# Performance work log

Hardware: AMD Instinct MI355X
Metric: run time of the kernel (lower is better)

The kernel has to match this reference:

```python
import jax, jax.numpy as jnp
import numpy as np

N_LAYERS = 3


def setup_inputs() -> dict:
    key = jax.random.key(0)
    k1, k2, k3, k4 = jax.random.split(key, 4)
    user_emb = jax.random.normal(k1, (29858, 64), dtype=jnp.float32)
    item_emb = jax.random.normal(k2, (40981, 64), dtype=jnp.float32)
    v = jax.random.normal(k3, (70839, 512), dtype=jnp.float32)
    filters = jax.random.normal(k4, (N_LAYERS, 512), dtype=jnp.float32)
    return {"user_emb": user_emb, "item_emb": item_emb, "v": v, "filters": filters}


def reference(user_emb, item_emb, v, filters):
    # ego: [N, D], v: [N, F], filters: [L, F]
    n_users = user_emb.shape[0]
    ego = jnp.concatenate([user_emb, item_emb], axis=0)
    acc = ego  # running sum for the mean over (layers + 1) embeddings
    for k in range(filters.shape[0]):
        # V @ diag(f) @ V^T @ ego  ==  V @ (f[:, None] * (V^T @ ego))
        proj = v.T @ ego                      # [F, D]
        ego = v @ (filters[k][:, None] * proj)  # [N, D]
        acc = acc + ego
    all_emb = acc / (filters.shape[0] + 1)
    return all_emb[:n_users], all_emb[n_users:]
```

## Files before the change

kernel.cpp:

```cpp
#include <hip/hip_runtime.h>
#include <hip/hip_bf16.h>


#define N_USERS 29858
#define N_TOTAL 70839
#define DQ 64
#define FD 512
#define NPAD 71168

typedef __attribute__((ext_vector_type(8))) short short8;
typedef __attribute__((ext_vector_type(4))) short short4v;
typedef __attribute__((ext_vector_type(4))) float f32x4;
typedef unsigned int u32;
typedef unsigned short u16;

static __device__ __forceinline__ u32 f32u(float x){union{float f;u32 u;}a;a.f=x;return a.u;}
static __device__ __forceinline__ float uf32(u32 u){union{u32 u;float f;}a;a.u=u;return a.f;}
static __device__ __forceinline__ u32 pack_h(u32 x0, u32 x1){
  return __builtin_amdgcn_perm(x1, x0, 0x07060302u);
}
static __device__ __forceinline__ void split_pair(u32 x0, u32 x1, u32& hp, u32& lp) {
  hp = pack_h(x0, x1);
  u32 l0 = f32u(uf32(x0) - uf32(x0 & 0xFFFF0000u));
  u32 l1 = f32u(uf32(x1) - uf32(x1 & 0xFFFF0000u));
  lp = pack_h(l0, l1);
}
union U8x { u32 u[4]; short8 s; };

static __device__ __forceinline__ u16 bf16_rne(float x) {
  u32 u = f32u(x);
  return (u16)((u + 0x7FFFu + ((u >> 16) & 1u)) >> 16);
}
static __device__ __forceinline__ void split2(float x, u16& h, u16& l) {
  h = bf16_rne(x);
  l = bf16_rne(x - uf32(((u32)h) << 16));
}

static __device__ __forceinline__ void load_lds16(const float* g, float* l) {
  __builtin_amdgcn_global_load_lds(
      (const __attribute__((address_space(1))) u32*)(g),
      (__attribute__((address_space(3))) u32*)(l), 16, 0, 0);
}


__global__ __launch_bounds__(256) void init_kernel(
    const float* __restrict__ u, const float* __restrict__ it,
    float* __restrict__ out, u16* __restrict__ egoTb) {
  __shared__ float tile[64][65];
  const int n0 = blockIdx.x * 64;
  const int t = threadIdx.x;
  const int r = t >> 2, cbase = (t & 3) * 16;
  {
    int n = n0 + r;
    if (n < N_TOTAL) {
      const float* src = (n < N_USERS) ? (u + (size_t)n * DQ)
                                       : (it + (size_t)(n - N_USERS) * DQ);
#pragma unroll
      for (int q = 0; q < 4; ++q) {
        f32x4 val = *(const f32x4*)(src + cbase + q * 4);
        *(f32x4*)(out + (size_t)n * DQ + cbase + q * 4) = val;
        tile[r][cbase + q * 4 + 0] = val[0];
        tile[r][cbase + q * 4 + 1] = val[1];
        tile[r][cbase + q * 4 + 2] = val[2];
        tile[r][cbase + q * 4 + 3] = val[3];
      }
    } else {
#pragma unroll
      for (int q = 0; q < 4; ++q)
#pragma unroll
        for (int e = 0; e < 4; ++e) tile[r][cbase + q * 4 + e] = 0.f;
    }
  }
  __syncthreads();
  const int s = t;
  const int d = (s & 15) | ((s >> 6) << 4);
  const int nb = (s >> 4) & 3;
#pragma unroll
  for (int sl = 0; sl < 2; ++sl) {
    U8x H, L;
#pragma unroll
    for (int j = 0; j < 4; ++j) {
      u16 h0, l0, h1, l1;
      split2(tile[sl * 32 + nb * 8 + 2 * j][d], h0, l0);
      split2(tile[sl * 32 + nb * 8 + 2 * j + 1][d], h1, l1);
      H.u[j] = (u32)h0 | ((u32)h1 << 16);
      L.u[j] = (u32)l0 | ((u32)l1 << 16);
    }
    size_t base = (size_t)(blockIdx.x * 2 + sl) * 4096;
    *(short8*)(egoTb + base + (size_t)s * 8) = H.s;
    *(short8*)(egoTb + base + 2048 + (size_t)s * 8) = L.s;
  }
}

__global__ __launch_bounds__(256, 3) void gram_kernel(
    const float* __restrict__ v, const u16* __restrict__ egoTb,
    float* __restrict__ parts, int chunk) {
  __shared__ short8 HAh[1024];
  __shared__ short8 HAl[1024];
  __shared__ short8 HBh[256];
  __shared__ short8 HBl[256];

  const int lid = blockIdx.x;
  const int cidx = (lid & 7) + 8 * ((lid >> 3) / 14);
  const int job = (lid >> 3) % 14;
  const int n0c = cidx * chunk;
  if (n0c >= NPAD) return;
  const int nend = min(n0c + chunk, NPAD);
  const bool isC0 = (job >= 12);
  const int itile = isC0 ? (job - 12) : (job < 8 ? 0 : 1);
  const int fA = itile * 256;
  const int jcol = isC0 ? 0 : (job < 8 ? job : job - 4);
  const int colbase = jcol * 64;
  const bool reuseB = !isC0 && (colbase >= fA) && (colbase + 64 <= fA + 256);
  const bool stageB = !isC0 && !reuseB;
  const int cb0q = reuseB ? ((colbase - fA) >> 6) : 0;

  const int t = threadIdx.x;
  const int lane = t & 63, wv = t >> 6;
  const int m16 = lane & 15, quad = lane >> 4;
  const int fl = lane, nq = wv;

  f32x4 acc[4][4];
#pragma unroll
  for (int a = 0; a < 4; ++a)
#pragma unroll
    for (int b = 0; b < 4; ++b) acc[a][b] = (f32x4){0.f, 0.f, 0.f, 0.f};

  u32 xA[4][8];
  u32 xB[8];
  short8 xBh, xBl;

  auto issue = [&](int n0) {
    if (isC0) {
      xBh = *(const short8*)(egoTb + (size_t)(n0 >> 5) * 4096 + (size_t)t * 8);
      xBl = *(const short8*)(egoTb + (size_t)(n0 >> 5) * 4096 + 2048 + (size_t)t * 8);
    }
#pragma unroll
    for (int seg = 0; seg < 4; ++seg)
#pragma unroll
      for (int r = 0; r < 8; ++r) {
        int n = n0 + nq * 8 + r;
        xA[seg][r] = (n < N_TOTAL) ? f32u(v[(size_t)n * FD + fA + seg * 64 + fl]) : 0u;
      }
    if (stageB) {
#pragma unroll
      for (int r = 0; r < 8; ++r) {
        int n = n0 + nq * 8 + r;
        xB[r] = (n < N_TOTAL) ? f32u(v[(size_t)n * FD + colbase + fl]) : 0u;
      }
    }
  };

  issue(n0c);

  for (int n0 = n0c; n0 < nend; n0 += 32) {
    asm volatile("s_barrier" ::: "memory");

    const int uw = (fl & 15) + ((fl >> 4) & 3) * 64 + nq * 16;
#pragma unroll
    for (int seg = 0; seg < 4; ++seg) {
      U8x H, L;
#pragma unroll
      for (int p = 0; p < 4; ++p)
        split_pair(xA[seg][2 * p], xA[seg][2 * p + 1], H.u[p], L.u[p]);
      HAh[uw + seg * 256] = H.s;
      HAl[uw + seg * 256] = L.s;
    }
    if (stageB) {
      U8x H, L;
#pragma unroll
      for (int p = 0; p < 4; ++p)
        split_pair(xB[2 * p], xB[2 * p + 1], H.u[p], L.u[p]);
      HBh[uw] = H.s;
      HBl[uw] = L.s;
    } else if (isC0) {
      HBh[t] = xBh;
      HBl[t] = xBl;
    }

    if (n0 + 32 < nend) issue(n0 + 32);

    asm volatile("s_waitcnt lgkmcnt(0)" ::: "memory");
    asm volatile("s_barrier" ::: "memory");

    short8 ah[4], al[4];
#pragma unroll
    for (int mt = 0; mt < 4; ++mt) {
      int u = m16 + mt * 64 + wv * 256 + quad * 16;
      ah[mt] = HAh[u];
      al[mt] = HAl[u];
    }
#pragma unroll
    for (int ct = 0; ct < 4; ++ct) {
      short8 bh, bl;
      if (reuseB) {
        int u = m16 + ct * 64 + cb0q * 256 + quad * 16;
        bh = HAh[u]; bl = HAl[u];
      } else {
        int u = m16 + ct * 64 + quad * 16;
        bh = HBh[u]; bl = HBl[u];
      }
#pragma unroll
      for (int mt = 0; mt < 4; ++mt) {
        acc[mt][ct] = __builtin_amdgcn_mfma_f32_16x16x32_bf16(ah[mt], bh, acc[mt][ct], 0, 0, 0);
        acc[mt][ct] = __builtin_amdgcn_mfma_f32_16x16x32_bf16(ah[mt], bl, acc[mt][ct], 0, 0, 0);
        acc[mt][ct] = __builtin_amdgcn_mfma_f32_16x16x32_bf16(al[mt], bh, acc[mt][ct], 0, 0, 0);
      }
    }
  }

  float* pb = parts + (size_t)cidx * (512 * 576);
  const int cb = isC0 ? 512 : colbase;
#pragma unroll
  for (int mt = 0; mt < 4; ++mt) {
    int row = fA + wv * 64 + mt * 16 + quad * 4;
#pragma unroll
    for (int ct = 0; ct < 4; ++ct) {
      int col = cb + ct * 16 + m16;
#pragma unroll
      for (int reg = 0; reg < 4; ++reg)
        pb[(size_t)(row + reg) * 576 + col] = acc[mt][ct][reg];
    }
  }
}

__global__ __launch_bounds__(256) void finalize_kernel(
    const float* __restrict__ parts, int nc,
    float* __restrict__ G, float* __restrict__ c0) {
  int idx = blockIdx.x * 256 + threadIdx.x;
  int r = idx / 576, c = idx % 576;
  float s = 0.f;
  if (c >= 512) {
    for (int p = 0; p < nc; ++p) s += parts[(size_t)p * (512 * 576) + r * 576 + c];
    c0[r * 64 + (c - 512)] = s;
  } else {
    bool direct = (c >> 6) >= 4 * (r >> 8);
    int rr = direct ? r : c, cc = direct ? c : r;
    for (int p = 0; p < nc; ++p) s += parts[(size_t)p * (512 * 576) + rr * 576 + cc];
    G[r * 512 + c] = s;
  }
}

__global__ __launch_bounds__(256) void apply_g_kernel(
    const float* __restrict__ G, const float* __restrict__ filt,
    const float* __restrict__ cin, float* __restrict__ cout) {
  __shared__ float red[4][64];
  const int t = threadIdx.x;
  const int i = blockIdx.x;
  const int sub = t >> 6, d = t & 63;
  float s = 0.f;
#pragma unroll 8
  for (int j = sub * 128; j < (sub + 1) * 128; ++j)
    s += G[i * 512 + j] * (filt[j] * cin[j * 64 + d]);
  red[sub][d] = s;
  __syncthreads();
  if (sub == 0)
    cout[i * 64 + d] = red[0][d] + red[1][d] + red[2][d] + red[3][d];
}

__global__ __launch_bounds__(256) void prep_wt_kernel(
    const float* __restrict__ filters, const float* __restrict__ c0,
    const float* __restrict__ c1, const float* __restrict__ c2,
    u16* __restrict__ wt_h) {
  int idx = blockIdx.x * 256 + threadIdx.x;
  int d = idx >> 9, f = idx & 511;
  float w = filters[f] * c0[f * 64 + d] + filters[512 + f] * c1[f * 64 + d] +
            filters[1024 + f] * c2[f * 64 + d];
  wt_h[d * FD + f] = bf16_rne(w);
}

__global__ __launch_bounds__(256) void expand_kernel(
    const float* __restrict__ v, const u16* __restrict__ wt_h,
    float* __restrict__ out) {
  __shared__ float raw[2][128 * 64];
  const int t = threadIdx.x;
  const int lane = t & 63, wv = t >> 6;
  const int m16 = lane & 15, quad = lane >> 4;
  const int nb = blockIdx.x * 128;

  f32x4 acc[2][4];
#pragma unroll
  for (int a = 0; a < 2; ++a)
#pragma unroll
    for (int b = 0; b < 4; ++b) acc[a][b] = (f32x4){0.f, 0.f, 0.f, 0.f};

  auto stage = [&](int buf, int fs) {
#pragma unroll
    for (int g = 0; g < 8; ++g) {
      int rl = g * 4 + (lane >> 4);
      int sw = rl & 7;
      int grow = min(nb + wv * 32 + rl, N_TOTAL - 1);
      const float* gp = v + (size_t)grow * FD + fs + (((lane & 15) ^ sw) << 2);
      load_lds16(gp, &raw[buf][(wv * 32 + g * 4) * 64]);
    }
  };

  stage(0, 0);
  for (int it8 = 0; it8 < 8; ++it8) {
    const int buf = it8 & 1, fs = it8 * 64;
    short8 pbh[2][4];
#pragma unroll
    for (int k = 0; k < 2; ++k)
#pragma unroll
      for (int ct = 0; ct < 4; ++ct) {
        const size_t off = (size_t)(ct * 16 + m16) * FD + fs + k * 32 + quad * 8;
        pbh[k][ct] = *(const short8*)(wt_h + off);
      }
    asm volatile("" ::: "memory");
    if (it8 + 1 < 8) {
      stage(buf ^ 1, fs + 64);
      asm volatile("s_waitcnt vmcnt(16)" ::: "memory");
    } else {
      asm volatile("s_waitcnt vmcnt(8)" ::: "memory");
    }
#pragma unroll
    for (int k0i = 0; k0i < 2; ++k0i) {
      short8 ah[2];
#pragma unroll
      for (int mt = 0; mt < 2; ++mt) {
        const float* rb = &raw[buf][(wv * 32 + mt * 16 + m16) * 64];
        const int sw = m16 & 7;
        const int j0 = k0i * 8 + quad * 2;
        f32x4 xa = *(const f32x4*)(rb + ((j0 ^ sw) << 2));
        f32x4 xb = *(const f32x4*)(rb + (((j0 + 1) ^ sw) << 2));
        U8x H;
        H.u[0] = pack_h(f32u(xa[0]), f32u(xa[1]));
        H.u[1] = pack_h(f32u(xa[2]), f32u(xa[3]));
        H.u[2] = pack_h(f32u(xb[0]), f32u(xb[1]));
        H.u[3] = pack_h(f32u(xb[2]), f32u(xb[3]));
        ah[mt] = H.s;
      }
#pragma unroll
      for (int ct = 0; ct < 4; ++ct) {
#pragma unroll
        for (int mt = 0; mt < 2; ++mt) {
          acc[mt][ct] = __builtin_amdgcn_mfma_f32_16x16x32_bf16(ah[mt], pbh[k0i][ct], acc[mt][ct], 0, 0, 0);
        }
      }
    }
  }

#pragma unroll
  for (int mt = 0; mt < 2; ++mt) {
    int nrow = nb + wv * 32 + mt * 16 + quad * 4;
#pragma unroll
    for (int ct = 0; ct < 4; ++ct) {
      int d = ct * 16 + m16;
#pragma unroll
      for (int reg = 0; reg < 4; ++reg) {
        int n = nrow + reg;
        if (n < N_TOTAL) {
          float* op = out + (size_t)n * DQ + d;
          *op = (*op + acc[mt][ct][reg]) * 0.25f;
        }
      }
    }
  }
}

extern "C" void kernel_launch(void* const* d_in, const int* in_sizes, int n_in,
                              void* d_out, int out_size, void* d_ws, size_t ws_size,
                              hipStream_t stream) {
  const float* user_emb = (const float*)d_in[0];
  const float* item_emb = (const float*)d_in[1];
  const float* v        = (const float*)d_in[2];
  const float* filters  = (const float*)d_in[3];
  float* out = (float*)d_out;

  const size_t EGOTB_BYTES = (size_t)(NPAD / 32) * 8192;
  const size_t SMALL_BYTES = (512 * 512 + 3 * 512 * 64) * 4 + DQ * FD * 2;
  size_t avail = ws_size > EGOTB_BYTES + SMALL_BYTES
                     ? ws_size - EGOTB_BYTES - SMALL_BYTES : 0;
  int nc = (int)(avail / ((size_t)512 * 576 * 4));
  if (nc > 35) nc = 35;
  if (nc < 1) nc = 1;
  int chunk = ((NPAD + nc - 1) / nc + 31) & ~31;
  int ncA = (NPAD + chunk - 1) / chunk;

  u16* egoTb  = (u16*)d_ws;
  float* parts = (float*)((char*)d_ws + EGOTB_BYTES);
  float* G     = parts + (size_t)ncA * 512 * 576;
  float* c0    = G + 512 * 512;
  float* c1    = c0 + 512 * 64;
  float* c2    = c1 + 512 * 64;
  u16* wt_h    = (u16*)(c2 + 512 * 64);

  int gblocks = 8 * 14 * ((ncA + 7) / 8);

  init_kernel<<<NPAD / 64, 256, 0, stream>>>(user_emb, item_emb, out, egoTb);
  gram_kernel<<<gblocks, 256, 0, stream>>>(v, egoTb, parts, chunk);
  finalize_kernel<<<(512 * 576) / 256, 256, 0, stream>>>(parts, ncA, G, c0);
  apply_g_kernel<<<512, 256, 0, stream>>>(G, filters, c0, c1);
  apply_g_kernel<<<512, 256, 0, stream>>>(G, filters + 512, c1, c2);
  prep_wt_kernel<<<128, 256, 0, stream>>>(filters, c0, c1, c2, wt_h);
  expand_kernel<<<NPAD / 128, 256, 0, stream>>>(v, wt_h, out);
}
```

Before: 486.8 us.

## Presplit V into bf16 hi/lo tiles once before the Gram kernel

Adds a presplit kernel that converts V once into bf16 high and low halves, stored in the MFMA-ready tiled layout. The Gram kernel then loads those tiles with vector loads instead of redoing scalar fp32 loads and splits for every job. This removes redundant split ALU work and the strided scalar loads, since each V segment was read by several jobs. In exchange it writes and reads an extra pass over a 2-byte-per-element copy of V (about 146MB total), needs a large workspace (falling back to the old path otherwise), and changes the grid mapping and occupancy hint.

```diff
diff --git a/kernel.cpp b/kernel.cpp
--- a/kernel.cpp
+++ b/kernel.cpp
@@ -9,7 +9,6 @@
 #define NPAD 71168
 
 typedef __attribute__((ext_vector_type(8))) short short8;
-typedef __attribute__((ext_vector_type(4))) short short4v;
 typedef __attribute__((ext_vector_type(4))) float f32x4;
 typedef unsigned int u32;
 typedef unsigned short u16;
@@ -72,9 +71,8 @@
     }
   }
   __syncthreads();
-  const int s = t;
-  const int d = (s & 15) | ((s >> 6) << 4);
-  const int nb = (s >> 4) & 3;
+  const int d = (t & 15) | ((t >> 6) << 4);
+  const int nb = (t >> 4) & 3;
 #pragma unroll
   for (int sl = 0; sl < 2; ++sl) {
     U8x H, L;
@@ -87,24 +85,67 @@
       L.u[j] = (u32)l0 | ((u32)l1 << 16);
     }
     size_t base = (size_t)(blockIdx.x * 2 + sl) * 4096;
-    *(short8*)(egoTb + base + (size_t)s * 8) = H.s;
-    *(short8*)(egoTb + base + 2048 + (size_t)s * 8) = L.s;
-  }
-}
-
-__global__ __launch_bounds__(256, 3) void gram_kernel(
-    const float* __restrict__ v, const u16* __restrict__ egoTb,
-    float* __restrict__ parts, int chunk) {
+    *(short8*)(egoTb + base + (size_t)t * 8) = H.s;
+    *(short8*)(egoTb + base + 2048 + (size_t)t * 8) = L.s;
+  }
+}
+
+__global__ __launch_bounds__(256) void presplit_kernel(
+    const float* __restrict__ v, u16* __restrict__ vbh, u16* __restrict__ vbl) {
+  __shared__ float tile[64][65];
+  const int n0 = blockIdx.x * 64;
+  const int t = threadIdx.x;
+  const int r = t >> 2, cbase = (t & 3) * 16;
+  const int d = (t & 15) | ((t >> 6) << 4);
+  const int nb = (t >> 4) & 3;
+  for (int fo = 0; fo < FD; fo += 64) {
+    __syncthreads();
+    {
+      int n = n0 + r;
+      if (n < N_TOTAL) {
+        const float* src = v + (size_t)n * FD + fo;
+#pragma unroll
+        for (int q = 0; q < 4; ++q) {
+          f32x4 val = *(const f32x4*)(src + cbase + q * 4);
+          tile[r][cbase + q * 4 + 0] = val[0];
+          tile[r][cbase + q * 4 + 1] = val[1];
+          tile[r][cbase + q * 4 + 2] = val[2];
+          tile[r][cbase + q * 4 + 3] = val[3];
+        }
+      } else {
+#pragma unroll
+        for (int q = 0; q < 4; ++q)
+#pragma unroll
+          for (int e = 0; e < 4; ++e) tile[r][cbase + q * 4 + e] = 0.f;
+      }
+    }
+    __syncthreads();
+#pragma unroll
+    for (int sl = 0; sl < 2; ++sl) {
+      U8x H, L;
+#pragma unroll
+      for (int j = 0; j < 4; ++j) {
+        u32 x0 = f32u(tile[sl * 32 + nb * 8 + 2 * j][d]);
+        u32 x1 = f32u(tile[sl * 32 + nb * 8 + 2 * j + 1][d]);
+        split_pair(x0, x1, H.u[j], L.u[j]);
+      }
+      size_t T = (size_t)((n0 >> 5) + sl) * 8 + (fo >> 6);
+      *(short8*)(vbh + T * 2048 + (size_t)t * 8) = H.s;
+      *(short8*)(vbl + T * 2048 + (size_t)t * 8) = L.s;
+    }
+  }
+}
+
+__global__ __launch_bounds__(256, 2) void gram_fast_kernel(
+    const u16* __restrict__ vbh, const u16* __restrict__ vbl,
+    const u16* __restrict__ egoTb, float* __restrict__ parts, int chunk) {
   __shared__ short8 HAh[1024];
   __shared__ short8 HAl[1024];
   __shared__ short8 HBh[256];
   __shared__ short8 HBl[256];
 
-  const int lid = blockIdx.x;
-  const int cidx = (lid & 7) + 8 * ((lid >> 3) / 14);
-  const int job = (lid >> 3) % 14;
-  const int n0c = cidx * chunk;
-  if (n0c >= NPAD) return;
+  const int job = blockIdx.x;
+  const int n0c = blockIdx.y * chunk;
   const int nend = min(n0c + chunk, NPAD);
   const bool isC0 = (job >= 12);
   const int itile = isC0 ? (job - 12) : (job < 8 ? 0 : 1);
@@ -118,7 +159,7 @@
   const int t = threadIdx.x;
   const int lane = t & 63, wv = t >> 6;
   const int m16 = lane & 15, quad = lane >> 4;
-  const int fl = lane, nq = wv;
+  const int ftA = fA >> 6;
 
   f32x4 acc[4][4];
 #pragma unroll
@@ -126,28 +167,23 @@
 #pragma unroll
     for (int b = 0; b < 4; ++b) acc[a][b] = (f32x4){0.f, 0.f, 0.f, 0.f};
 
-  u32 xA[4][8];
-  u32 xB[8];
-  short8 xBh, xBl;
+  short8 xAh[4], xAl[4], xBh, xBl;
 
   auto issue = [&](int n0) {
+    size_t Tb = (size_t)(n0 >> 5) * 8;
     if (isC0) {
       xBh = *(const short8*)(egoTb + (size_t)(n0 >> 5) * 4096 + (size_t)t * 8);
       xBl = *(const short8*)(egoTb + (size_t)(n0 >> 5) * 4096 + 2048 + (size_t)t * 8);
-    }
-#pragma unroll
-    for (int seg = 0; seg < 4; ++seg)
-#pragma unroll
-      for (int r = 0; r < 8; ++r) {
-        int n = n0 + nq * 8 + r;
-        xA[seg][r] = (n < N_TOTAL) ? f32u(v[(size_t)n * FD + fA + seg * 64 + fl]) : 0u;
-      }
-    if (stageB) {
-#pragma unroll
-      for (int r = 0; r < 8; ++r) {
-        int n = n0 + nq * 8 + r;
-        xB[r] = (n < N_TOTAL) ? f32u(v[(size_t)n * FD + colbase + fl]) : 0u;
-      }
+    } else if (stageB) {
+      size_t base = (Tb + (colbase >> 6)) * 2048 + (size_t)t * 8;
+      xBh = *(const short8*)(vbh + base);
+      xBl = *(const short8*)(vbl + base);
+    }
+#pragma unroll
+    for (int seg = 0; seg < 4; ++seg) {
+      size_t base = (Tb + ftA + seg) * 2048 + (size_t)t * 8;
+      xAh[seg] = *(const short8*)(vbh + base);
+      xAl[seg] = *(const short8*)(vbl + base);
     }
   };
 
@@ -156,24 +192,12 @@
   for (int n0 = n0c; n0 < nend; n0 += 32) {
     asm volatile("s_barrier" ::: "memory");
 
-    const int uw = (fl & 15) + ((fl >> 4) & 3) * 64 + nq * 16;
 #pragma unroll
     for (int seg = 0; seg < 4; ++seg) {
-      U8x H, L;
-#pragma unroll
-      for (int p = 0; p < 4; ++p)
-        split_pair(xA[seg][2 * p], xA[seg][2 * p + 1], H.u[p], L.u[p]);
-      HAh[uw + seg * 256] = H.s;
-      HAl[uw + seg * 256] = L.s;
-    }
-    if (stageB) {
-      U8x H, L;
-#pragma unroll
-      for (int p = 0; p < 4; ++p)
-        split_pair(xB[2 * p], xB[2 * p + 1], H.u[p], L.u[p]);
-      HBh[uw] = H.s;
-      HBl[uw] = L.s;
-    } else if (isC0) {
+      HAh[seg * 256 + t] = xAh[seg];
+      HAl[seg * 256 + t] = xAl[seg];
+    }
+    if (stageB || isC0) {
       HBh[t] = xBh;
       HBl[t] = xBl;
     }
@@ -209,7 +233,136 @@
     }
   }
 
-  float* pb = parts + (size_t)cidx * (512 * 576);
+  float* pb = parts + (size_t)blockIdx.y * (512 * 576);
+  const int cb = isC0 ? 512 : colbase;
+#pragma unroll
+  for (int mt = 0; mt < 4; ++mt) {
+    int row = fA + wv * 64 + mt * 16 + quad * 4;
+#pragma unroll
+    for (int ct = 0; ct < 4; ++ct) {
+      int col = cb + ct * 16 + m16;
+#pragma unroll
+      for (int reg = 0; reg < 4; ++reg)
+        pb[(size_t)(row + reg) * 576 + col] = acc[mt][ct][reg];
+    }
+  }
+}
+
+__global__ __launch_bounds__(256, 2) void gram_split_kernel(
+    const float* __restrict__ v, const u16* __restrict__ egoTb,
+    float* __restrict__ parts, int chunk) {
+  __shared__ short8 HAh[1024];
+  __shared__ short8 HAl[1024];
+  __shared__ short8 HBh[256];
+  __shared__ short8 HBl[256];
+
+  const int job = blockIdx.x;
+  const int n0c = blockIdx.y * chunk;
+  const int nend = min(n0c + chunk, NPAD);
+  const bool isC0 = (job >= 12);
+  const int itile = isC0 ? (job - 12) : (job < 8 ? 0 : 1);
+  const int fA = itile * 256;
+  const int jcol = isC0 ? 0 : (job < 8 ? job : job - 4);
+  const int colbase = jcol * 64;
+  const bool reuseB = !isC0 && (colbase >= fA) && (colbase + 64 <= fA + 256);
+  const bool stageB = !isC0 && !reuseB;
+  const int cb0q = reuseB ? ((colbase - fA) >> 6) : 0;
+
+  const int t = threadIdx.x;
+  const int lane = t & 63, wv = t >> 6;
+  const int m16 = lane & 15, quad = lane >> 4;
+  const int fl = lane, nq = wv;
+
+  f32x4 acc[4][4];
+#pragma unroll
+  for (int a = 0; a < 4; ++a)
+#pragma unroll
+    for (int b = 0; b < 4; ++b) acc[a][b] = (f32x4){0.f, 0.f, 0.f, 0.f};
+
+  u32 xA[4][8];
+  u32 xB[8];
+  short8 xBh, xBl;
+
+  auto issue = [&](int n0) {
+    if (isC0) {
+      xBh = *(const short8*)(egoTb + (size_t)(n0 >> 5) * 4096 + (size_t)t * 8);
+      xBl = *(const short8*)(egoTb + (size_t)(n0 >> 5) * 4096 + 2048 + (size_t)t * 8);
+    }
+#pragma unroll
+    for (int seg = 0; seg < 4; ++seg)
+#pragma unroll
+      for (int r = 0; r < 8; ++r) {
+        int n = n0 + nq * 8 + r;
+        xA[seg][r] = (n < N_TOTAL) ? f32u(v[(size_t)n * FD + fA + seg * 64 + fl]) : 0u;
+      }
+    if (stageB) {
+#pragma unroll
+      for (int r = 0; r < 8; ++r) {
+        int n = n0 + nq * 8 + r;
+        xB[r] = (n < N_TOTAL) ? f32u(v[(size_t)n * FD + colbase + fl]) : 0u;
+      }
+    }
+  };
+
+  issue(n0c);
+
+  for (int n0 = n0c; n0 < nend; n0 += 32) {
+    asm volatile("s_barrier" ::: "memory");
+
+    const int uw = (fl & 15) + ((fl >> 4) & 3) * 64 + nq * 16;
+#pragma unroll
+    for (int seg = 0; seg < 4; ++seg) {
+      U8x H, L;
+#pragma unroll
+      for (int p = 0; p < 4; ++p)
+        split_pair(xA[seg][2 * p], xA[seg][2 * p + 1], H.u[p], L.u[p]);
+      HAh[uw + seg * 256] = H.s;
+      HAl[uw + seg * 256] = L.s;
+    }
+    if (stageB) {
+      U8x H, L;
+#pragma unroll
+      for (int p = 0; p < 4; ++p)
+        split_pair(xB[2 * p], xB[2 * p + 1], H.u[p], L.u[p]);
+      HBh[uw] = H.s;
+      HBl[uw] = L.s;
+    } else if (isC0) {
+      HBh[t] = xBh;
+      HBl[t] = xBl;
+    }
+
+    if (n0 + 32 < nend) issue(n0 + 32);
+
+    asm volatile("s_waitcnt lgkmcnt(0)" ::: "memory");
+    asm volatile("s_barrier" ::: "memory");
+
+    short8 ah[4], al[4];
+#pragma unroll
+    for (int mt = 0; mt < 4; ++mt) {
+      int u = m16 + mt * 64 + wv * 256 + quad * 16;
+      ah[mt] = HAh[u];
+      al[mt] = HAl[u];
+    }
+#pragma unroll
+    for (int ct = 0; ct < 4; ++ct) {
+      short8 bh, bl;
+      if (reuseB) {
+        int u = m16 + ct * 64 + cb0q * 256 + quad * 16;
+        bh = HAh[u]; bl = HAl[u];
+      } else {
+        int u = m16 + ct * 64 + quad * 16;
+        bh = HBh[u]; bl = HBl[u];
+      }
+#pragma unroll
+      for (int mt = 0; mt < 4; ++mt) {
+        acc[mt][ct] = __builtin_amdgcn_mfma_f32_16x16x32_bf16(ah[mt], bh, acc[mt][ct], 0, 0, 0);
+        acc[mt][ct] = __builtin_amdgcn_mfma_f32_16x16x32_bf16(ah[mt], bl, acc[mt][ct], 0, 0, 0);
+        acc[mt][ct] = __builtin_amdgcn_mfma_f32_16x16x32_bf16(al[mt], bh, acc[mt][ct], 0, 0, 0);
+      }
+    }
+  }
+
+  float* pb = parts + (size_t)blockIdx.y * (512 * 576);
   const int cb = isC0 ? 512 : colbase;
 #pragma unroll
   for (int mt = 0; mt < 4; ++mt) {
@@ -331,12 +484,10 @@
         ah[mt] = H.s;
       }
 #pragma unroll
-      for (int ct = 0; ct < 4; ++ct) {
-#pragma unroll
-        for (int mt = 0; mt < 2; ++mt) {
+      for (int ct = 0; ct < 4; ++ct)
+#pragma unroll
+        for (int mt = 0; mt < 2; ++mt)
           acc[mt][ct] = __builtin_amdgcn_mfma_f32_16x16x32_bf16(ah[mt], pbh[k0i][ct], acc[mt][ct], 0, 0, 0);
-        }
-      }
     }
   }
 
@@ -368,27 +519,45 @@
   float* out = (float*)d_out;
 
   const size_t EGOTB_BYTES = (size_t)(NPAD / 32) * 8192;
+  const size_t VB_BYTES    = (size_t)NPAD * FD * 2;
   const size_t SMALL_BYTES = (512 * 512 + 3 * 512 * 64) * 4 + DQ * FD * 2;
-  size_t avail = ws_size > EGOTB_BYTES + SMALL_BYTES
-                     ? ws_size - EGOTB_BYTES - SMALL_BYTES : 0;
-  int nc = (int)(avail / ((size_t)512 * 576 * 4));
-  if (nc > 35) nc = 35;
-  if (nc < 1) nc = 1;
+  const size_t PART_BYTES  = (size_t)512 * 576 * 4;
+
+  size_t fixed_fast = EGOTB_BYTES + 2 * VB_BYTES + SMALL_BYTES;
+  int nc_fast = ws_size > fixed_fast ? (int)((ws_size - fixed_fast) / PART_BYTES) : 0;
+  const bool fast = (nc_fast >= 28);
+
+  int nc;
+  if (fast) {
+    nc = nc_fast > 35 ? 35 : nc_fast;
+  } else {
+    size_t fixed = EGOTB_BYTES + SMALL_BYTES;
+    size_t avail = ws_size > fixed ? ws_size - fixed : 0;
+    nc = (int)(avail / PART_BYTES);
+    if (nc > 35) nc = 35;
+    if (nc < 1) nc = 1;
+  }
   int chunk = ((NPAD + nc - 1) / nc + 31) & ~31;
   int ncA = (NPAD + chunk - 1) / chunk;
 
-  u16* egoTb  = (u16*)d_ws;
-  float* parts = (float*)((char*)d_ws + EGOTB_BYTES);
-  float* G     = parts + (size_t)ncA * 512 * 576;
-  float* c0    = G + 512 * 512;
-  float* c1    = c0 + 512 * 64;
-  float* c2    = c1 + 512 * 64;
-  u16* wt_h    = (u16*)(c2 + 512 * 64);
-
-  int gblocks = 8 * 14 * ((ncA + 7) / 8);
+  char* p = (char*)d_ws;
+  u16* egoTb = (u16*)p;            p += EGOTB_BYTES;
+  u16* vbh = nullptr; u16* vbl = nullptr;
+  if (fast) { vbh = (u16*)p; p += VB_BYTES; vbl = (u16*)p; p += VB_BYTES; }
+  float* parts = (float*)p;        p += (size_t)ncA * PART_BYTES;
+  float* G     = (float*)p;        p += (size_t)512 * 512 * 4;
+  float* c0    = (float*)p;        p += (size_t)512 * 64 * 4;
+  float* c1    = (float*)p;        p += (size_t)512 * 64 * 4;
+  float* c2    = (float*)p;        p += (size_t)512 * 64 * 4;
+  u16* wt_h    = (u16*)p;
 
   init_kernel<<<NPAD / 64, 256, 0, stream>>>(user_emb, item_emb, out, egoTb);
-  gram_kernel<<<gblocks, 256, 0, stream>>>(v, egoTb, parts, chunk);
+  if (fast) {
+    presplit_kernel<<<NPAD / 64, 256, 0, stream>>>(v, vbh, vbl);
+    gram_fast_kernel<<<dim3(14, ncA), 256, 0, stream>>>(vbh, vbl, egoTb, parts, chunk);
+  } else {
+    gram_split_kernel<<<dim3(14, ncA), 256, 0, stream>>>(v, egoTb, parts, chunk);
+  }
   finalize_kernel<<<(512 * 576) / 256, 256, 0, stream>>>(parts, ncA, G, c0);
   apply_g_kernel<<<512, 256, 0, stream>>>(G, filters, c0, c1);
   apply_g_kernel<<<512, 256, 0, stream>>>(G, filters + 512, c1, c2);
```

New measurement: 511.1 us. +5.0%, slower.
